# Performance work log

Hardware: AMD Instinct MI355X
Metric: run time of the kernel (lower is better)

## Reference

```python
import jax, jax.numpy as jnp
import numpy as np

N = 8192
IN_F = 256
OUT_F = 128
E = 262144
ALPHA = 0.2  # LeakyReLU negative slope
NEG_INF = -9e15


def setup_inputs() -> dict:
    key = jax.random.key(0)
    k_h, k_e, k_w, k_bl, k_a, k_ba = jax.random.split(key, 6)
    h = jax.random.normal(k_h, (N, IN_F), dtype=jnp.float32)
    edge_index = jax.random.randint(k_e, (2, E), 0, N, dtype=jnp.int64)
    # nn.Linear(in_features, out_features): weight [out, in], bias [out]
    lim_w = 1.0 / np.sqrt(IN_F)
    W = jax.random.uniform(k_w, (OUT_F, IN_F), minval=-lim_w, maxval=lim_w, dtype=jnp.float32)
    b_lin = jax.random.uniform(k_bl, (OUT_F,), minval=-lim_w, maxval=lim_w, dtype=jnp.float32)
    # nn.Linear(2*out_features, 1): weight [1, 2*out], bias [1]
    lim_a = 1.0 / np.sqrt(2 * OUT_F)
    a = jax.random.uniform(k_a, (1, 2 * OUT_F), minval=-lim_a, maxval=lim_a, dtype=jnp.float32)
    b_att = jax.random.uniform(k_ba, (1,), minval=-lim_a, maxval=lim_a, dtype=jnp.float32)
    return {"h": h, "edge_index": edge_index, "W": W, "b_lin": b_lin, "a": a, "b_att": b_att}


def reference(h, edge_index, W, b_lin, a, b_att):
    n = h.shape[0]
    Wh = h @ W.T + b_lin  # [N, F_out]
    # a . [Wh_i || Wh_j] + b == Wh_i.a1 + Wh_j.a2 + b  (exact decomposition of the
    # concat-pairwise attention linear; avoids materializing [N, N, 2F])
    a1 = a[0, :OUT_F]
    a2 = a[0, OUT_F:]
    s1 = Wh @ a1  # [N]
    s2 = Wh @ a2  # [N]
    e = jax.nn.leaky_relu(s1[:, None] + s2[None, :] + b_att[0], negative_slope=ALPHA)  # [N, N]
    # dense adjacency mask from edge_index (to_dense_adj semantics)
    adj = jnp.zeros((n, n), dtype=jnp.float32).at[edge_index[0], edge_index[1]].set(1.0)
    attention = jnp.where(adj > 0, e, jnp.float32(NEG_INF))
    attention = jax.nn.softmax(attention, axis=1)
    h_prime = attention @ Wh  # [N, F_out]
    return jax.nn.elu(h_prime)
```

## Files before the change

kernel.cpp:

```cpp
#include <hip/hip_runtime.h>
#include <hip/hip_bf16.h>
#include <math.h>

#define N_NODES 8192
#define IN_FEAT 256
#define OUT_FEAT 128
#define NUM_E 262144
#define LRELU_ALPHA 0.2f
#define CAP 128

typedef __bf16 bf16x8 __attribute__((ext_vector_type(8)));
typedef float f32x4 __attribute__((ext_vector_type(4)));

__global__ __launch_bounds__(256) void k_gemm(const float* __restrict__ h,
                                              const float* __restrict__ W,
                                              const float* __restrict__ b_lin,
                                              const float* __restrict__ a_att,
                                              const float* __restrict__ b_att,
                                              __hip_bfloat16* __restrict__ Whb,
                                              float* __restrict__ s1,
                                              float* __restrict__ s2,
                                              int* __restrict__ deg) {
    const int tid = threadIdx.x;
    if (tid < 32) deg[blockIdx.x * 32 + tid] = 0;

    const int lane = tid & 63;
    const int w    = tid >> 6;
    const int m    = lane & 15;
    const int quad = lane >> 4;
    const int r0   = blockIdx.x * 32;
    const int wrow = r0 + (w & 1) * 16;
    const int wcol = (w >> 1) * 64;

    f32x4 acc[4] = {};

    const float* hrow = h + (wrow + m) * IN_FEAT + quad * 8;
    #pragma unroll
    for (int ks = 0; ks < 8; ++ks) {
        const int k = ks * 32;
        float4 ha = *(const float4*)(hrow + k);
        float4 hb = *(const float4*)(hrow + k + 4);
        bf16x8 af;
        af[0] = (__bf16)ha.x; af[1] = (__bf16)ha.y; af[2] = (__bf16)ha.z; af[3] = (__bf16)ha.w;
        af[4] = (__bf16)hb.x; af[5] = (__bf16)hb.y; af[6] = (__bf16)hb.z; af[7] = (__bf16)hb.w;
        #pragma unroll
        for (int nt = 0; nt < 4; ++nt) {
            const float* wp = W + (wcol + nt * 16 + m) * IN_FEAT + quad * 8 + k;
            float4 wa = *(const float4*)(wp);
            float4 wb = *(const float4*)(wp + 4);
            bf16x8 bfv;
            bfv[0] = (__bf16)wa.x; bfv[1] = (__bf16)wa.y; bfv[2] = (__bf16)wa.z; bfv[3] = (__bf16)wa.w;
            bfv[4] = (__bf16)wb.x; bfv[5] = (__bf16)wb.y; bfv[6] = (__bf16)wb.z; bfv[7] = (__bf16)wb.w;
            acc[nt] = __builtin_amdgcn_mfma_f32_16x16x32_bf16(af, bfv, acc[nt], 0, 0, 0);
        }
    }

    float p1[4] = {0.f, 0.f, 0.f, 0.f};
    float p2[4] = {0.f, 0.f, 0.f, 0.f};
    #pragma unroll
    for (int nt = 0; nt < 4; ++nt) {
        const int col = wcol + nt * 16 + m;
        const float bl = b_lin[col];
        const float a1 = a_att[col];
        const float a2 = a_att[OUT_FEAT + col];
        #pragma unroll
        for (int reg = 0; reg < 4; ++reg) {
            const float v = acc[nt][reg] + bl;
            const int row = wrow + quad * 4 + reg;
            Whb[row * OUT_FEAT + col] = __float2bfloat16(v);
            p1[reg] = fmaf(v, a1, p1[reg]);
            p2[reg] = fmaf(v, a2, p2[reg]);
        }
    }
    #pragma unroll
    for (int off = 1; off < 16; off <<= 1) {
        #pragma unroll
        for (int reg = 0; reg < 4; ++reg) {
            p1[reg] += __shfl_xor(p1[reg], off, 64);
            p2[reg] += __shfl_xor(p2[reg], off, 64);
        }
    }
    __shared__ float red1[32][2];
    __shared__ float red2[32][2];
    if (m == 0) {
        #pragma unroll
        for (int reg = 0; reg < 4; ++reg) {
            const int rl = (w & 1) * 16 + quad * 4 + reg;
            red1[rl][w >> 1] = p1[reg];
            red2[rl][w >> 1] = p2[reg];
        }
    }
    __syncthreads();
    if (tid < 32) {
        s1[r0 + tid] = red1[tid][0] + red1[tid][1] + b_att[0];
    } else if (tid < 64) {
        const int r = tid - 32;
        s2[r0 + r] = red2[r][0] + red2[r][1];
    }
}

__global__ __launch_bounds__(256) void k_scatter(const int* __restrict__ ei,
                                                 int* __restrict__ deg,
                                                 int* __restrict__ elist) {
    const int k = blockIdx.x * blockDim.x + threadIdx.x;
    if (k >= NUM_E) return;
    const int r = ei[k];
    const int c = ei[NUM_E + k];
    const int p = atomicAdd(&deg[r], 1);
    if (p < CAP) elist[r * CAP + p] = c;
}

__global__ __launch_bounds__(128) void k_aggr(const int* __restrict__ deg,
                                              const int* __restrict__ elist,
                                              const float* __restrict__ s1,
                                              const float* __restrict__ s2,
                                              const __hip_bfloat16* __restrict__ Whb,
                                              float* __restrict__ out) {
    __shared__ float el[CAP];
    __shared__ int   jl[CAP];
    __shared__ float sred[2];
    __shared__ float colred[2][128];
    const int tid = threadIdx.x;
    const int w = tid >> 6, lane = tid & 63;
    const int i = blockIdx.x;

    int n = deg[i]; n = n < CAP ? n : CAP;
    const float s1i = s1[i];

    if (tid < n) jl[tid] = elist[i * CAP + tid];
    __syncthreads();

    float e = -3.0e38f;
    bool valid = false;
    if (tid < n) {
        const int j = jl[tid];
        valid = true;
        for (int s = 0; s < tid; ++s)
            if (jl[s] == j) { valid = false; break; }
        if (valid) {
            float v = s1i + s2[j];
            v = v > 0.f ? v : LRELU_ALPHA * v;
            e = v;
        }
    }
    float mx = e;
    #pragma unroll
    for (int off = 32; off > 0; off >>= 1) mx = fmaxf(mx, __shfl_xor(mx, off, 64));
    if (lane == 0) sred[w] = mx;
    __syncthreads();
    const float mval = fmaxf(sred[0], sred[1]);
    __syncthreads();

    const float wt = valid ? __expf(e - mval) : 0.f;
    if (tid < n) el[tid] = wt;
    float ls = wt;
    #pragma unroll
    for (int off = 32; off > 0; off >>= 1) ls += __shfl_xor(ls, off, 64);
    if (lane == 0) sred[w] = ls;
    __syncthreads();
    const float denom = sred[0] + sred[1];

    const unsigned int* W2 = (const unsigned int*)Whb;
    float ax = 0.f, ay = 0.f;
    for (int t = w; t < n; t += 2) {
        const float wv = el[t];
        const unsigned int u = W2[jl[t] * (OUT_FEAT / 2) + lane];
        union { unsigned int ui; float f; } lo, hi;
        lo.ui = u << 16;
        hi.ui = u & 0xffff0000u;
        ax = fmaf(wv, lo.f, ax);
        ay = fmaf(wv, hi.f, ay);
    }
    colred[w][lane * 2]     = ax;
    colred[w][lane * 2 + 1] = ay;
    __syncthreads();

    float o;
    if (n > 0) {
        o = (colred[0][tid] + colred[1][tid]) / denom;
    } else {
        float acc = 0.f;
        for (int r = 0; r < N_NODES; ++r) acc += __bfloat162float(Whb[r * OUT_FEAT + tid]);
        o = acc * (1.f / (float)N_NODES);
    }
    out[i * OUT_FEAT + tid] = o > 0.f ? o : expm1f(o);
}

extern "C" void kernel_launch(void* const* d_in, const int* in_sizes, int n_in,
                              void* d_out, int out_size, void* d_ws, size_t ws_size,
                              hipStream_t stream) {
    const float* h     = (const float*)d_in[0];
    const int*   ei    = (const int*)d_in[1];
    const float* W     = (const float*)d_in[2];
    const float* b_lin = (const float*)d_in[3];
    const float* a     = (const float*)d_in[4];
    const float* b_att = (const float*)d_in[5];
    float* out = (float*)d_out;

    char* ws = (char*)d_ws;
    __hip_bfloat16* Whb = (__hip_bfloat16*)(ws);
    float* s1    = (float*)(ws + 2097152);
    float* s2    = (float*)(ws + 2097152 + 32768);
    int*   elist = (int*)(ws + 2097152 + 65536);
    int*   deg   = (int*)(ws + 2097152 + 65536 + 4194304);

    k_gemm<<<N_NODES / 32, 256, 0, stream>>>(h, W, b_lin, a, b_att, Whb, s1, s2, deg);
    k_scatter<<<NUM_E / 256, 256, 0, stream>>>(ei, deg, elist);
    k_aggr<<<N_NODES, 128, 0, stream>>>(deg, elist, s1, s2, Whb, out);
}
```

Before: 117.4 us.

## Retile GEMM, vectorize scatter, bitmap dedup and split-row aggregation

The GEMM now gives each block 16 rows instead of 32, doubling the block count, with each of four waves covering 32 output columns. The scatter kernel has each thread load four edges with int4 and issue four atomics. The aggregation kernel replaces the quadratic duplicate-neighbour scan with a shared-memory bitmap and atomicOr, and splits neighbours across four half-wave slots, each reading 8 bytes per lane. This aims to cut the O(n^2) dedup cost and raise parallelism and memory-level concurrency, at the price of clearing a 1KB bitmap per block and more shared-memory reduction.

```diff
diff --git a/kernel.cpp b/kernel.cpp
--- a/kernel.cpp
+++ b/kernel.cpp
@@ -8,6 +8,7 @@
 #define NUM_E 262144
 #define LRELU_ALPHA 0.2f
 #define CAP 128
+#define BM_W 256
 
 typedef __bf16 bf16x8 __attribute__((ext_vector_type(8)));
 typedef float f32x4 __attribute__((ext_vector_type(4)));
@@ -22,19 +23,18 @@
                                               float* __restrict__ s2,
                                               int* __restrict__ deg) {
     const int tid = threadIdx.x;
-    if (tid < 32) deg[blockIdx.x * 32 + tid] = 0;
+    if (tid < 16) deg[blockIdx.x * 16 + tid] = 0;
 
     const int lane = tid & 63;
     const int w    = tid >> 6;
     const int m    = lane & 15;
     const int quad = lane >> 4;
-    const int r0   = blockIdx.x * 32;
-    const int wrow = r0 + (w & 1) * 16;
-    const int wcol = (w >> 1) * 64;
-
-    f32x4 acc[4] = {};
-
-    const float* hrow = h + (wrow + m) * IN_FEAT + quad * 8;
+    const int r0   = blockIdx.x * 16;
+    const int wcol = w * 32;
+
+    f32x4 acc[2] = {};
+
+    const float* hrow = h + (r0 + m) * IN_FEAT + quad * 8;
     #pragma unroll
     for (int ks = 0; ks < 8; ++ks) {
         const int k = ks * 32;
@@ -44,7 +44,7 @@
         af[0] = (__bf16)ha.x; af[1] = (__bf16)ha.y; af[2] = (__bf16)ha.z; af[3] = (__bf16)ha.w;
         af[4] = (__bf16)hb.x; af[5] = (__bf16)hb.y; af[6] = (__bf16)hb.z; af[7] = (__bf16)hb.w;
         #pragma unroll
-        for (int nt = 0; nt < 4; ++nt) {
+        for (int nt = 0; nt < 2; ++nt) {
             const float* wp = W + (wcol + nt * 16 + m) * IN_FEAT + quad * 8 + k;
             float4 wa = *(const float4*)(wp);
             float4 wb = *(const float4*)(wp + 4);
@@ -58,7 +58,7 @@
     float p1[4] = {0.f, 0.f, 0.f, 0.f};
     float p2[4] = {0.f, 0.f, 0.f, 0.f};
     #pragma unroll
-    for (int nt = 0; nt < 4; ++nt) {
+    for (int nt = 0; nt < 2; ++nt) {
         const int col = wcol + nt * 16 + m;
         const float bl = b_lin[col];
         const float a1 = a_att[col];
@@ -66,7 +66,7 @@
         #pragma unroll
         for (int reg = 0; reg < 4; ++reg) {
             const float v = acc[nt][reg] + bl;
-            const int row = wrow + quad * 4 + reg;
+            const int row = r0 + quad * 4 + reg;
             Whb[row * OUT_FEAT + col] = __float2bfloat16(v);
             p1[reg] = fmaf(v, a1, p1[reg]);
             p2[reg] = fmaf(v, a2, p2[reg]);
@@ -80,34 +80,36 @@
             p2[reg] += __shfl_xor(p2[reg], off, 64);
         }
     }
-    __shared__ float red1[32][2];
-    __shared__ float red2[32][2];
+    __shared__ float red1[16][4];
+    __shared__ float red2[16][4];
     if (m == 0) {
         #pragma unroll
         for (int reg = 0; reg < 4; ++reg) {
-            const int rl = (w & 1) * 16 + quad * 4 + reg;
-            red1[rl][w >> 1] = p1[reg];
-            red2[rl][w >> 1] = p2[reg];
-        }
-    }
-    __syncthreads();
-    if (tid < 32) {
-        s1[r0 + tid] = red1[tid][0] + red1[tid][1] + b_att[0];
-    } else if (tid < 64) {
-        const int r = tid - 32;
-        s2[r0 + r] = red2[r][0] + red2[r][1];
+            red1[quad * 4 + reg][w] = p1[reg];
+            red2[quad * 4 + reg][w] = p2[reg];
+        }
+    }
+    __syncthreads();
+    if (tid < 16) {
+        s1[r0 + tid] = red1[tid][0] + red1[tid][1] + red1[tid][2] + red1[tid][3] + b_att[0];
+    } else if (tid >= 64 && tid < 80) {
+        const int r = tid - 64;
+        s2[r0 + r] = red2[r][0] + red2[r][1] + red2[r][2] + red2[r][3];
     }
 }
 
 __global__ __launch_bounds__(256) void k_scatter(const int* __restrict__ ei,
                                                  int* __restrict__ deg,
                                                  int* __restrict__ elist) {
-    const int k = blockIdx.x * blockDim.x + threadIdx.x;
-    if (k >= NUM_E) return;
-    const int r = ei[k];
-    const int c = ei[NUM_E + k];
-    const int p = atomicAdd(&deg[r], 1);
-    if (p < CAP) elist[r * CAP + p] = c;
+    const int k4 = (blockIdx.x * 256 + threadIdx.x) * 4;
+    if (k4 >= NUM_E) return;
+    const int4 r = *(const int4*)&ei[k4];
+    const int4 c = *(const int4*)&ei[NUM_E + k4];
+    int p;
+    p = atomicAdd(&deg[r.x], 1); if (p < CAP) elist[r.x * CAP + p] = c.x;
+    p = atomicAdd(&deg[r.y], 1); if (p < CAP) elist[r.y * CAP + p] = c.y;
+    p = atomicAdd(&deg[r.z], 1); if (p < CAP) elist[r.z * CAP + p] = c.z;
+    p = atomicAdd(&deg[r.w], 1); if (p < CAP) elist[r.w * CAP + p] = c.w;
 }
 
 __global__ __launch_bounds__(128) void k_aggr(const int* __restrict__ deg,
@@ -116,27 +118,29 @@
                                               const float* __restrict__ s2,
                                               const __hip_bfloat16* __restrict__ Whb,
                                               float* __restrict__ out) {
+    __shared__ unsigned int bm[BM_W];
     __shared__ float el[CAP];
     __shared__ int   jl[CAP];
     __shared__ float sred[2];
-    __shared__ float colred[2][128];
+    __shared__ float colred[4][128];
     const int tid = threadIdx.x;
     const int w = tid >> 6, lane = tid & 63;
     const int i = blockIdx.x;
 
+    bm[tid] = 0u; bm[tid + 128] = 0u;
+    __syncthreads();
+
     int n = deg[i]; n = n < CAP ? n : CAP;
     const float s1i = s1[i];
-
-    if (tid < n) jl[tid] = elist[i * CAP + tid];
-    __syncthreads();
 
     float e = -3.0e38f;
     bool valid = false;
     if (tid < n) {
-        const int j = jl[tid];
-        valid = true;
-        for (int s = 0; s < tid; ++s)
-            if (jl[s] == j) { valid = false; break; }
+        const int j = elist[i * CAP + tid];
+        jl[tid] = j;
+        const unsigned int bit = 1u << (j & 31);
+        const unsigned int old = atomicOr(&bm[j >> 5], bit);
+        valid = !(old & bit);
         if (valid) {
             float v = s1i + s2[j];
             v = v > 0.f ? v : LRELU_ALPHA * v;
@@ -160,24 +164,31 @@
     __syncthreads();
     const float denom = sred[0] + sred[1];
 
-    const unsigned int* W2 = (const unsigned int*)Whb;
-    float ax = 0.f, ay = 0.f;
-    for (int t = w; t < n; t += 2) {
+    const int half = lane >> 5;
+    const int cb = (lane & 31) * 4;
+    float a0 = 0.f, a1 = 0.f, a2 = 0.f, a3 = 0.f;
+    for (int t = w * 2 + half; t < n; t += 4) {
         const float wv = el[t];
-        const unsigned int u = W2[jl[t] * (OUT_FEAT / 2) + lane];
-        union { unsigned int ui; float f; } lo, hi;
-        lo.ui = u << 16;
-        hi.ui = u & 0xffff0000u;
-        ax = fmaf(wv, lo.f, ax);
-        ay = fmaf(wv, hi.f, ay);
-    }
-    colred[w][lane * 2]     = ax;
-    colred[w][lane * 2 + 1] = ay;
+        const int j = jl[t];
+        const uint2 u = *(const uint2*)&Whb[j * OUT_FEAT + cb];
+        union { unsigned int ui; float f; } c0, c1, c2, c3;
+        c0.ui = u.x << 16; c1.ui = u.x & 0xffff0000u;
+        c2.ui = u.y << 16; c3.ui = u.y & 0xffff0000u;
+        a0 = fmaf(wv, c0.f, a0);
+        a1 = fmaf(wv, c1.f, a1);
+        a2 = fmaf(wv, c2.f, a2);
+        a3 = fmaf(wv, c3.f, a3);
+    }
+    const int slot = w * 2 + half;
+    colred[slot][cb]     = a0;
+    colred[slot][cb + 1] = a1;
+    colred[slot][cb + 2] = a2;
+    colred[slot][cb + 3] = a3;
     __syncthreads();
 
     float o;
     if (n > 0) {
-        o = (colred[0][tid] + colred[1][tid]) / denom;
+        o = (colred[0][tid] + colred[1][tid] + colred[2][tid] + colred[3][tid]) / denom;
     } else {
         float acc = 0.f;
         for (int r = 0; r < N_NODES; ++r) acc += __bfloat162float(Whb[r * OUT_FEAT + tid]);
@@ -204,7 +215,7 @@
     int*   elist = (int*)(ws + 2097152 + 65536);
     int*   deg   = (int*)(ws + 2097152 + 65536 + 4194304);
 
-    k_gemm<<<N_NODES / 32, 256, 0, stream>>>(h, W, b_lin, a, b_att, Whb, s1, s2, deg);
-    k_scatter<<<NUM_E / 256, 256, 0, stream>>>(ei, deg, elist);
+    k_gemm<<<N_NODES / 16, 256, 0, stream>>>(h, W, b_lin, a, b_att, Whb, s1, s2, deg);
+    k_scatter<<<NUM_E / 1024, 256, 0, stream>>>(ei, deg, elist);
     k_aggr<<<N_NODES, 128, 0, stream>>>(deg, elist, s1, s2, Whb, out);
 }
```

Result: faster. 105.4 us (-10.2%).
